# Optimization experiments

Hardware: AMD Instinct MI355X
Metric: run time of the kernel (lower is better)

The kernel has to match this reference:

```python
import jax, jax.numpy as jnp
import numpy as np

G = 8          # groups
EPS = 1e-5     # GroupNorm eps

def maxpool(x, k):
    pad = k // 2
    return jax.lax.reduce_window(x, -jnp.inf, jax.lax.max,
                                 (1, 1, k, k), (1, 1, 1, 1),
                                 [(0, 0), (0, 0), (pad, pad), (pad, pad)])

def conv1x1(x, w):
    # w: [out, in], x: [B, in, H, W]
    return jnp.einsum('oi,bihw->bohw', w, x)

def setup_inputs() -> dict:
    key = jax.random.key(0)
    ks = jax.random.split(key, 8)
    B, Cin, H, W = 16, 256, 64, 64
    planes = 256
    s = 0.05
    return {
        'x': jax.random.normal(ks[0], (B, Cin, H, W), jnp.float32),
        'mask': jax.random.uniform(ks[1], (B, 2, H, W), jnp.float32),
        'Wt': jax.random.normal(ks[2], (planes, Cin), jnp.float32) * s,
        'Wtm': jax.random.normal(ks[3], (1, 2), jnp.float32) * s,
        'Wp': jax.random.normal(ks[4], (planes // 2, Cin), jnp.float32) * s,
        'Wg': jax.random.normal(ks[5], (planes // 2, Cin), jnp.float32) * s,
        'Wz': jax.random.normal(ks[6], (G, Cin // G, planes // G), jnp.float32) * s,
        'gamma': jnp.ones((Cin,), jnp.float32),
        'beta': jnp.zeros((Cin,), jnp.float32),
    }

def reference(x, mask, Wt, Wtm, Wp, Wg, Wz, gamma, beta):
    B, Cin, H, W = x.shape
    planes = Wt.shape[0]
    cg = planes // G
    HW = H * W

    t = conv1x1(x, Wt)                      # [B, planes, H, W]
    t_mask = conv1x1(mask, Wtm)             # [B, 1, H, W]
    t = t * t_mask + t

    p = conv1x1(x, Wp)                      # [B, planes//2, H, W]
    p = jnp.concatenate([p, maxpool(p, 3), maxpool(p, 5)], axis=1)
    g = conv1x1(x, Wg)
    g = jnp.concatenate([g, maxpool(g, 3), maxpool(g, 5)], axis=1)
    # torch.split(_, cg) + loop over `groups` consumes only the first `planes` channels
    p = p[:, :planes]
    g = g[:, :planes]

    # kernel(), vectorized over groups: softmax over spatial, global scalar att per group
    ts = jax.nn.softmax(t.reshape(B, G, cg, HW), axis=-1)        # softmax dim=2 of [b,c,hw]
    pf = p.reshape(B, G, cg * HW)
    gf = g.reshape(B, G, cg * HW)
    att = jnp.einsum('bgn,bgn->bg', pf, gf)                      # bmm([b,1,n],[b,n,1])
    xk = (att[:, :, None, None] * ts).reshape(B, planes, H, W)

    # grouped 1x1 conv z: planes -> inplanes with G groups
    xz = jnp.einsum('goi,bgihw->bgohw', Wz,
                    xk.reshape(B, G, cg, H, W)).reshape(B, Cin, H, W)

    # GroupNorm(G, Cin)
    xg = xz.reshape(B, G, -1)
    mu = xg.mean(-1, keepdims=True)
    var = xg.var(-1, keepdims=True)
    xn = ((xg - mu) * jax.lax.rsqrt(var + EPS)).reshape(B, Cin, H, W)
    xn = xn * gamma[None, :, None, None] + beta[None, :, None, None]

    return xn + x
```

## Files before the change

kernel.cpp:

```cpp
#include <hip/hip_runtime.h>
#include <math.h>

#define B_      16
#define CIN     256
#define HW_     4096
#define PLANES  256
#define G_      8
#define EPSV    1e-5f

typedef unsigned short u16;
typedef __attribute__((ext_vector_type(8))) short short8;
typedef __attribute__((ext_vector_type(4))) float f32x4;

__device__ inline u16 f2bf(float f) {
    union { float f; unsigned u; } v; v.f = f;
    unsigned u = v.u;
    return (u16)((u + 0x7fffu + ((u >> 16) & 1u)) >> 16);
}
__device__ inline float bf2f(u16 h) {
    union { unsigned u; float f; } v; v.u = ((unsigned)h) << 16;
    return v.f;
}

__global__ __launch_bounds__(256) void k_packA(
    const float* __restrict__ Wt, const float* __restrict__ Wp,
    const float* __restrict__ Wg,
    u16* __restrict__ pAhi, u16* __restrict__ pAlo)
{
    int t = blockIdx.x * 256 + threadIdx.x;
    int lane = t & 63;
    int mb   = (t >> 6) & 7;
    int kt   = (t >> 9) & 7;
    int rt   = (t >> 12) & 3;
    int row = rt * 128 + mb * 16 + (lane & 15);
    int k0  = kt * 32 + (lane >> 4) * 8;
    const float* src;
    if      (row < 256) src = Wt + (size_t)row * 256;
    else if (row < 384) src = Wp + (size_t)(row - 256) * 256;
    else                src = Wg + (size_t)(row - 384) * 256;
    u16 hv[8], lv[8];
    #pragma unroll
    for (int j = 0; j < 8; ++j) {
        float w = src[k0 + j];
        u16 h = f2bf(w);
        hv[j] = h;
        lv[j] = f2bf(w - bf2f(h));
    }
    *(short8*)(pAhi + (size_t)t * 8) = *(short8*)hv;
    *(short8*)(pAlo + (size_t)t * 8) = *(short8*)lv;
}

__global__ __launch_bounds__(256) void k_transpose(
    const float* __restrict__ x, u16* __restrict__ xThi,
    u16* __restrict__ xTlo)
{
    __shared__ float tile[32][129];
    int tid = threadIdx.x;
    int px0 = blockIdx.x * 128;
    int c0  = blockIdx.y * 32;
    int bg  = blockIdx.z;

    #pragma unroll
    for (int it = 0; it < 16; ++it) {
        int flat = it * 256 + tid;
        int c_l = flat >> 7, p_l = flat & 127;
        tile[c_l][p_l] = x[((size_t)bg * 256 + c0 + c_l) * 4096 + px0 + p_l];
    }
    __syncthreads();
    #pragma unroll
    for (int it = 0; it < 8; ++it) {
        int flat = it * 256 + tid;
        int p_l = flat >> 4;
        int c_l = (flat & 15) * 2;
        float v0 = tile[c_l][p_l], v1 = tile[c_l + 1][p_l];
        u16 h0 = f2bf(v0), h1 = f2bf(v1);
        u16 l0 = f2bf(v0 - bf2f(h0)), l1 = f2bf(v1 - bf2f(h1));
        size_t o = ((size_t)bg * 4096 + px0 + p_l) * 256 + c0 + c_l;
        u16 ho[2] = { h0, h1 };
        u16 lo[2] = { l0, l1 };
        *(unsigned*)(xThi + o) = *(unsigned*)ho;
        *(unsigned*)(xTlo + o) = *(unsigned*)lo;
    }
}

__global__ __launch_bounds__(256) void k_tmod_zero(
    const float* __restrict__ mask, const float* __restrict__ Wtm,
    float* __restrict__ tmod, float* __restrict__ att, float* __restrict__ stats)
{
    int idx = blockIdx.x * 256 + threadIdx.x;
    float w0 = Wtm[0], w1 = Wtm[1];
    if (idx < B_ * HW_) {
        int b = idx >> 12, pix = idx & 4095;
        const float* mb = mask + (size_t)b * 2 * HW_;
        tmod[idx] = 1.0f + w0 * mb[pix] + w1 * mb[HW_ + pix];
    }
    if (blockIdx.x == 0) {
        if (threadIdx.x < 128) att[threadIdx.x] = 0.0f;
        stats[threadIdx.x] = 0.0f;
    }
}

#define STAGE16(SRC)                                                          \
    _Pragma("unroll")                                                         \
    for (int it = 0; it < 16; ++it) {                                         \
        int cidx = it * 256 + tid;                                            \
        int px   = cidx >> 5;                                                 \
        int boff = (cidx & 31) << 4;                                          \
        short8 v = *(const short8*)((SRC) + (size_t)px * 512 + boff);         \
        *(short8*)(Blds + px * 512 + (boff ^ ((px & 7) << 4))) = v;           \
    }

#define MFMA_PASS(ABASE)                                                      \
    _Pragma("unroll")                                                         \
    for (int kt = 0; kt < 8; ++kt) {                                          \
        short8 a[4], bb[4];                                                   \
        _Pragma("unroll")                                                     \
        for (int m = 0; m < 4; ++m)                                           \
            a[m] = *(const short8*)((ABASE) + kt * 8192 + m * 1024);          \
        int off = ((kt * 64) + ((lane >> 4) << 4)) ^ ((lane & 7) << 4);       \
        _Pragma("unroll")                                                     \
        for (int n = 0; n < 4; ++n) {                                         \
            int px = wn * 64 + n * 16 + (lane & 15);                          \
            bb[n] = *(const short8*)(Blds + px * 512 + off);                  \
        }                                                                     \
        _Pragma("unroll")                                                     \
        for (int m = 0; m < 4; ++m)                                           \
            _Pragma("unroll")                                                 \
            for (int n = 0; n < 4; ++n)                                       \
                acc[m][n] = __builtin_amdgcn_mfma_f32_16x16x32_bf16(          \
                    a[m], bb[n], acc[m][n], 0, 0, 0);                         \
    }

#define MFMA_PASS2(AH, AL)                                                    \
    _Pragma("unroll")                                                         \
    for (int kt = 0; kt < 8; ++kt) {                                          \
        short8 ah[4], al[4], bb[4];                                           \
        _Pragma("unroll")                                                     \
        for (int m = 0; m < 4; ++m) {                                         \
            ah[m] = *(const short8*)((AH) + kt * 8192 + m * 1024);            \
            al[m] = *(const short8*)((AL) + kt * 8192 + m * 1024);            \
        }                                                                     \
        int off = ((kt * 64) + ((lane >> 4) << 4)) ^ ((lane & 7) << 4);       \
        _Pragma("unroll")                                                     \
        for (int n = 0; n < 4; ++n) {                                         \
            int px = wn * 64 + n * 16 + (lane & 15);                          \
            bb[n] = *(const short8*)(Blds + px * 512 + off);                  \
        }                                                                     \
        _Pragma("unroll")                                                     \
        for (int m = 0; m < 4; ++m)                                           \
            _Pragma("unroll")                                                 \
            for (int n = 0; n < 4; ++n) {                                     \
                acc[m][n] = __builtin_amdgcn_mfma_f32_16x16x32_bf16(          \
                    ah[m], bb[n], acc[m][n], 0, 0, 0);                        \
                acc[m][n] = __builtin_amdgcn_mfma_f32_16x16x32_bf16(          \
                    al[m], bb[n], acc[m][n], 0, 0, 0);                        \
            }                                                                 \
    }

__global__ __launch_bounds__(256) void k_mm0(
    const u16* __restrict__ xThi, const u16* __restrict__ pAhi,
    const float* __restrict__ tmod, u16* __restrict__ tbuf)
{
    __shared__ short8 BldsV[4096];
    char* Blds = (char*)BldsV;
    int tid = threadIdx.x, lane = tid & 63, wid = tid >> 6;
    int wm = wid >> 1, wn = wid & 1;
    int pix0 = blockIdx.x * 128;
    int rt   = blockIdx.y;
    int bg   = blockIdx.z;

    const char* srcHi = (const char*)(xThi + ((size_t)bg * 4096 + pix0) * 256);
    const char* aHi = (const char*)pAhi + rt * 65536 + wm * 4096 + lane * 16;

    f32x4 acc[4][4];
    #pragma unroll
    for (int m = 0; m < 4; ++m)
        #pragma unroll
        for (int n = 0; n < 4; ++n) acc[m][n] = (f32x4)0.0f;

    STAGE16(srcHi);
    __syncthreads();
    MFMA_PASS(aHi);

    int colb = pix0 + wn * 64;
    int rowb = rt * 128 + wm * 64;
    float tm[4];
    #pragma unroll
    for (int n = 0; n < 4; ++n) tm[n] = tmod[bg * 4096 + colb + n * 16 + (lane & 15)];
    #pragma unroll
    for (int m = 0; m < 4; ++m)
        #pragma unroll
        for (int n = 0; n < 4; ++n)
            #pragma unroll
            for (int r = 0; r < 4; ++r) {
                int row = rowb + m * 16 + (lane >> 4) * 4 + r;
                int col = colb + n * 16 + (lane & 15);
                tbuf[((size_t)bg * 256 + row) * 4096 + col] = f2bf(acc[m][n][r] * tm[n]);
            }
}

__global__ __launch_bounds__(256) void k_mm1(
    const u16* __restrict__ xThi, const u16* __restrict__ xTlo,
    const u16* __restrict__ pAhi, const u16* __restrict__ pAlo,
    float* __restrict__ pbuf, float* __restrict__ gbuf)
{
    __shared__ short8 BldsV[4096];
    char* Blds = (char*)BldsV;
    int tid = threadIdx.x, lane = tid & 63, wid = tid >> 6;
    int wm = wid >> 1, wn = wid & 1;
    int pix0 = blockIdx.x * 128;
    int by   = blockIdx.y;
    int bg   = blockIdx.z;

    const char* srcHi = (const char*)(xThi + ((size_t)bg * 4096 + pix0) * 256);
    const char* srcLo = (const char*)(xTlo + ((size_t)bg * 4096 + pix0) * 256);
    const char* aHi = (const char*)pAhi + (2 + by) * 65536 + wm * 4096 + lane * 16;
    const char* aLo = (const char*)pAlo + (2 + by) * 65536 + wm * 4096 + lane * 16;

    f32x4 acc[4][4];
    #pragma unroll
    for (int m = 0; m < 4; ++m)
        #pragma unroll
        for (int n = 0; n < 4; ++n) acc[m][n] = (f32x4)0.0f;

    STAGE16(srcHi);
    __syncthreads();
    MFMA_PASS2(aHi, aLo);
    __syncthreads();
    STAGE16(srcLo);
    __syncthreads();
    MFMA_PASS(aHi);

    float* dst = (by == 0) ? pbuf : gbuf;
    int colb = pix0 + wn * 64;
    int rowb = wm * 64;
    #pragma unroll
    for (int m = 0; m < 4; ++m)
        #pragma unroll
        for (int n = 0; n < 4; ++n)
            #pragma unroll
            for (int r = 0; r < 4; ++r) {
                int row = rowb + m * 16 + (lane >> 4) * 4 + r;
                int col = colb + n * 16 + (lane & 15);
                dst[((size_t)bg * 128 + row) * 4096 + col] = acc[m][n][r];
            }
}

__global__ __launch_bounds__(256) void k_att(
    const float* __restrict__ pbuf, const float* __restrict__ gbuf,
    float* __restrict__ att)
{
    __shared__ float hmp[HW_];
    __shared__ float hmg[HW_];
    __shared__ float halo[256][4];
    __shared__ float scr[8];
    int c  = blockIdx.x;
    int gi = blockIdx.y;
    int b  = blockIdx.z;
    int tid = threadIdx.x;
    int tq = tid & 3;
    int r  = tid >> 2;
    int px0 = tid * 16;

    const float* pp = pbuf + ((size_t)b * 128 + gi * 32 + c) * HW_ + px0;
    const float* gg = gbuf + ((size_t)b * 128 + gi * 32 + c) * HW_ + px0;

    float pv[16], gv[16];
    float racc = 0.0f;
    #pragma unroll
    for (int i = 0; i < 4; ++i) {
        float4 p4 = *(const float4*)(pp + i * 4);
        float4 g4 = *(const float4*)(gg + i * 4);
        pv[4*i+0] = p4.x; pv[4*i+1] = p4.y; pv[4*i+2] = p4.z; pv[4*i+3] = p4.w;
        gv[4*i+0] = g4.x; gv[4*i+1] = g4.y; gv[4*i+2] = g4.z; gv[4*i+3] = g4.w;
        racc += p4.x * g4.x + p4.y * g4.y + p4.z * g4.z + p4.w * g4.w;
    }
    halo[tid][0] = pv[0]; halo[tid][1] = pv[15];
    halo[tid][2] = gv[0]; halo[tid][3] = gv[15];
    __syncthreads();

    float pL = (tq > 0) ? halo[tid - 1][1] : pv[0];
    float pR = (tq < 3) ? halo[tid + 1][0] : pv[15];
    float gL = (tq > 0) ? halo[tid - 1][3] : gv[0];
    float gR = (tq < 3) ? halo[tid + 1][2] : gv[15];

    float hp[16], hg[16];
    hp[0] = fmaxf(fmaxf(pL, pv[0]), pv[1]);
    hg[0] = fmaxf(fmaxf(gL, gv[0]), gv[1]);
    #pragma unroll
    for (int j = 1; j < 15; ++j) {
        hp[j] = fmaxf(fmaxf(pv[j-1], pv[j]), pv[j+1]);
        hg[j] = fmaxf(fmaxf(gv[j-1], gv[j]), gv[j+1]);
    }
    hp[15] = fmaxf(fmaxf(pv[14], pv[15]), pR);
    hg[15] = fmaxf(fmaxf(gv[14], gv[15]), gR);

    #pragma unroll
    for (int i = 0; i < 4; ++i) {
        *(float4*)(&hmp[px0 + i * 4]) = make_float4(hp[4*i], hp[4*i+1], hp[4*i+2], hp[4*i+3]);
        *(float4*)(&hmg[px0 + i * 4]) = make_float4(hg[4*i], hg[4*i+1], hg[4*i+2], hg[4*i+3]);
    }
    __syncthreads();

    int up = (r > 0)  ? px0 - 64 : px0;
    int dn = (r < 63) ? px0 + 64 : px0;
    float pacc = 0.0f;
    #pragma unroll
    for (int i = 0; i < 4; ++i) {
        float4 pu = *(const float4*)(&hmp[up + i * 4]);
        float4 pd = *(const float4*)(&hmp[dn + i * 4]);
        float4 gu = *(const float4*)(&hmg[up + i * 4]);
        float4 gd = *(const float4*)(&hmg[dn + i * 4]);
        float mpx, mgx;
        mpx = fmaxf(fmaxf(pu.x, hp[4*i+0]), pd.x); mgx = fmaxf(fmaxf(gu.x, hg[4*i+0]), gd.x); pacc += mpx * mgx;
        mpx = fmaxf(fmaxf(pu.y, hp[4*i+1]), pd.y); mgx = fmaxf(fmaxf(gu.y, hg[4*i+1]), gd.y); pacc += mpx * mgx;
        mpx = fmaxf(fmaxf(pu.z, hp[4*i+2]), pd.z); mgx = fmaxf(fmaxf(gu.z, hg[4*i+2]), gd.z); pacc += mpx * mgx;
        mpx = fmaxf(fmaxf(pu.w, hp[4*i+3]), pd.w); mgx = fmaxf(fmaxf(gu.w, hg[4*i+3]), gd.w); pacc += mpx * mgx;
    }

    #pragma unroll
    for (int off = 32; off > 0; off >>= 1) {
        racc += __shfl_down(racc, off, 64);
        pacc += __shfl_down(pacc, off, 64);
    }
    int lane = tid & 63, wid = tid >> 6;
    if (lane == 0) { scr[wid] = racc; scr[4 + wid] = pacc; }
    __syncthreads();
    if (tid == 0) {
        atomicAdd(&att[b * 8 + gi],     scr[0] + scr[1] + scr[2] + scr[3]);
        atomicAdd(&att[b * 8 + gi + 4], scr[4] + scr[5] + scr[6] + scr[7]);
    }
}

__global__ __launch_bounds__(256) void k_smax(
    const u16* __restrict__ tbuf, float2* __restrict__ rowstat)
{
    __shared__ float scr[8];
    int r = blockIdx.x;
    const u16* tr = tbuf + (size_t)r * HW_;
    int tid = threadIdx.x;
    int lane = tid & 63, wid = tid >> 6;

    float vals[16];
    float mx = -3.0e38f;
    #pragma unroll
    for (int it = 0; it < 2; ++it) {
        short8 v = *(const short8*)(tr + it * 2048 + tid * 8);
        #pragma unroll
        for (int j = 0; j < 8; ++j) {
            float f = bf2f((u16)v[j]);
            vals[it * 8 + j] = f;
            mx = fmaxf(mx, f);
        }
    }
    #pragma unroll
    for (int off = 32; off > 0; off >>= 1) mx = fmaxf(mx, __shfl_down(mx, off, 64));
    if (lane == 0) scr[wid] = mx;
    __syncthreads();
    if (tid == 0) scr[0] = fmaxf(fmaxf(scr[0], scr[1]), fmaxf(scr[2], scr[3]));
    __syncthreads();
    float m = scr[0];
    __syncthreads();

    float s = 0.0f;
    #pragma unroll
    for (int j = 0; j < 16; ++j) s += __expf(vals[j] - m);
    #pragma unroll
    for (int off = 32; off > 0; off >>= 1) s += __shfl_down(s, off, 64);
    if (lane == 0) scr[4 + wid] = s;
    __syncthreads();
    if (tid == 0) {
        float S = scr[4] + scr[5] + scr[6] + scr[7];
        rowstat[r] = make_float2(m, 1.0f / S);
    }
}

__global__ __launch_bounds__(256) void k_xz2(
    u16* __restrict__ tbuf, const float* __restrict__ Wz,
    const float2* __restrict__ rowstat, const float* __restrict__ att,
    float* __restrict__ stats)
{
    __shared__ float wz[32][32];
    __shared__ float2 rs[32];
    __shared__ float scr[8];
    int pt  = blockIdx.x;
    int gi  = blockIdx.y;
    int b   = blockIdx.z;
    int tid = threadIdx.x;
    int px  = pt * 512 + tid * 2;

    const float* wzg = Wz + gi * 1024;
    #pragma unroll
    for (int i = 0; i < 4; ++i) {
        int idx = tid + i * 256;
        wz[idx >> 5][idx & 31] = wzg[idx];
    }
    if (tid < 32) rs[tid] = rowstat[b * 256 + gi * 32 + tid];
    __syncthreads();

    u16* base = tbuf + ((size_t)b * 256 + gi * 32) * HW_;
    float2 v[32];
    #pragma unroll
    for (int i = 0; i < 32; ++i) {
        unsigned rv = *(const unsigned*)(base + (size_t)i * HW_ + px);
        float m = rs[i].x, inv = rs[i].y;
        v[i].x = __expf(bf2f((u16)(rv & 0xffffu)) - m) * inv;
        v[i].y = __expf(bf2f((u16)(rv >> 16)) - m) * inv;
    }

    float a = att[b * 8 + gi];
    float s1 = 0.0f, s2 = 0.0f;
    #pragma unroll
    for (int o = 0; o < 32; ++o) {
        const float4* wzo = (const float4*)(&wz[o][0]);
        float ax = 0.0f, ay = 0.0f;
        #pragma unroll
        for (int j = 0; j < 8; ++j) {
            float4 w = wzo[j];
            ax = fmaf(w.x, v[4*j+0].x, ax); ay = fmaf(w.x, v[4*j+0].y, ay);
            ax = fmaf(w.y, v[4*j+1].x, ax); ay = fmaf(w.y, v[4*j+1].y, ay);
            ax = fmaf(w.z, v[4*j+2].x, ax); ay = fmaf(w.z, v[4*j+2].y, ay);
            ax = fmaf(w.w, v[4*j+3].x, ax); ay = fmaf(w.w, v[4*j+3].y, ay);
        }
        ax *= a; ay *= a;
        unsigned ov = (unsigned)f2bf(ax) | ((unsigned)f2bf(ay) << 16);
        *(unsigned*)(base + (size_t)o * HW_ + px) = ov;
        s1 += ax + ay;
        s2 = fmaf(ax, ax, fmaf(ay, ay, s2));
    }

    #pragma unroll
    for (int off = 32; off > 0; off >>= 1) {
        s1 += __shfl_down(s1, off, 64);
        s2 += __shfl_down(s2, off, 64);
    }
    int lane = tid & 63, wid = tid >> 6;
    if (lane == 0) { scr[wid] = s1; scr[4 + wid] = s2; }
    __syncthreads();
    if (tid == 0) {
        atomicAdd(&stats[(b * 8 + gi) * 2 + 0], scr[0] + scr[1] + scr[2] + scr[3]);
        atomicAdd(&stats[(b * 8 + gi) * 2 + 1], scr[4] + scr[5] + scr[6] + scr[7]);
    }
}

__global__ __launch_bounds__(256) void k_finalize(
    const u16* __restrict__ xzbuf, const float* __restrict__ x,
    const float* __restrict__ stats, const float* __restrict__ gamma,
    const float* __restrict__ beta, float* __restrict__ out)
{
    size_t i0 = ((size_t)blockIdx.x * 256 + threadIdx.x) * 4;
    int c  = (int)((i0 >> 12) & 255);
    int bg = (int)(i0 >> 17);
    float s1 = stats[bg * 2], s2 = stats[bg * 2 + 1];
    const float invN = 1.0f / 131072.0f;
    float mu  = s1 * invN;
    float var = s2 * invN - mu * mu;
    float rs  = rsqrtf(var + EPSV);
    float ga = gamma[c], be = beta[c];

    union { unsigned long long u; u16 h[4]; } vv;
    vv.u = *(const unsigned long long*)(xzbuf + i0);
    float4 xv = *(const float4*)(x + i0);
    float4 o;
    o.x = (bf2f(vv.h[0]) - mu) * rs * ga + be + xv.x;
    o.y = (bf2f(vv.h[1]) - mu) * rs * ga + be + xv.y;
    o.z = (bf2f(vv.h[2]) - mu) * rs * ga + be + xv.z;
    o.w = (bf2f(vv.h[3]) - mu) * rs * ga + be + xv.w;
    *(float4*)(out + i0) = o;
}

extern "C" void kernel_launch(void* const* d_in, const int* in_sizes, int n_in,
                              void* d_out, int out_size, void* d_ws, size_t ws_size,
                              hipStream_t stream)
{
    const float* x     = (const float*)d_in[0];
    const float* mask  = (const float*)d_in[1];
    const float* Wt    = (const float*)d_in[2];
    const float* Wtm   = (const float*)d_in[3];
    const float* Wp    = (const float*)d_in[4];
    const float* Wg    = (const float*)d_in[5];
    const float* Wz    = (const float*)d_in[6];
    const float* gamma = (const float*)d_in[7];
    const float* beta  = (const float*)d_in[8];
    float* out = (float*)d_out;

    char* ws = (char*)d_ws;
    u16*   tbuf  = (u16*)(ws);
    u16*   xThi  = (u16*)(ws + 33554432);
    u16*   xTlo  = (u16*)(ws + 67108864);
    float* pbuf  = (float*)(ws + 100663296);
    float* gbuf  = (float*)(ws + 167772160);
    u16*   pAhi  = (u16*)(ws + 234881024);
    u16*   pAlo  = (u16*)(ws + 235143168);
    float* tmod  = (float*)(ws + 235405312);
    float* att   = (float*)(ws + 235667456);
    float* stats = att + 128;
    float2* rowstat = (float2*)(ws + 235669504);

    k_packA    <<<64, 256, 0, stream>>>(Wt, Wp, Wg, pAhi, pAlo);
    k_tmod_zero<<<256, 256, 0, stream>>>(mask, Wtm, tmod, att, stats);
    k_transpose<<<dim3(32, 8, 16), 256, 0, stream>>>(x, xThi, xTlo);
    k_mm0      <<<dim3(32, 2, 16), 256, 0, stream>>>(xThi, pAhi, tmod, tbuf);
    k_mm1      <<<dim3(32, 2, 16), 256, 0, stream>>>(xThi, xTlo, pAhi, pAlo, pbuf, gbuf);
    k_att      <<<dim3(32, 4, 16), 256, 0, stream>>>(pbuf, gbuf, att);
    k_smax     <<<4096, 256, 0, stream>>>(tbuf, rowstat);
    k_xz2      <<<dim3(8, 8, 16), 256, 0, stream>>>(tbuf, Wz, rowstat, att, stats);
    k_finalize <<<16384, 256, 0, stream>>>(tbuf, x, stats, gamma, beta, out);
}
```

Measured before the change: 179.5 us.

## Fuse t and p/g projection GEMMs into one kernel sharing staged x tiles

Merges the two 1x1-conv GEMM kernels into a single kernel. Each block now stages a 64-pixel tile of both the hi and lo bf16 parts of x once and computes all three outputs from it: t (bf16, scaled by the mask modulation), p and g (fp32 via hi/lo split). This removes one launch and the repeated global reads of the x tiles across blocks and kernels. In exchange the grid becomes 1024 blocks with a smaller pixel tile, and each wave runs all three MFMA passes serially.

```diff
diff --git a/kernel.cpp b/kernel.cpp
--- a/kernel.cpp
+++ b/kernel.cpp
@@ -100,17 +100,17 @@
     }
 }
 
-#define STAGE16(SRC)                                                          \
+#define STAGE8(SRC, DST)                                                      \
     _Pragma("unroll")                                                         \
-    for (int it = 0; it < 16; ++it) {                                         \
+    for (int it = 0; it < 8; ++it) {                                          \
         int cidx = it * 256 + tid;                                            \
         int px   = cidx >> 5;                                                 \
         int boff = (cidx & 31) << 4;                                          \
         short8 v = *(const short8*)((SRC) + (size_t)px * 512 + boff);         \
-        *(short8*)(Blds + px * 512 + (boff ^ ((px & 7) << 4))) = v;           \
-    }
-
-#define MFMA_PASS(ABASE)                                                      \
+        *(short8*)((DST) + px * 512 + (boff ^ ((px & 7) << 4))) = v;          \
+    }
+
+#define MFMA_PASS_B(ABASE, BBASE)                                             \
     _Pragma("unroll")                                                         \
     for (int kt = 0; kt < 8; ++kt) {                                          \
         short8 a[4], bb[4];                                                   \
@@ -120,8 +120,8 @@
         int off = ((kt * 64) + ((lane >> 4) << 4)) ^ ((lane & 7) << 4);       \
         _Pragma("unroll")                                                     \
         for (int n = 0; n < 4; ++n) {                                         \
-            int px = wn * 64 + n * 16 + (lane & 15);                          \
-            bb[n] = *(const short8*)(Blds + px * 512 + off);                  \
+            int px = n * 16 + (lane & 15);                                    \
+            bb[n] = *(const short8*)((BBASE) + px * 512 + off);               \
         }                                                                     \
         _Pragma("unroll")                                                     \
         for (int m = 0; m < 4; ++m)                                           \
@@ -131,7 +131,7 @@
                     a[m], bb[n], acc[m][n], 0, 0, 0);                         \
     }
 
-#define MFMA_PASS2(AH, AL)                                                    \
+#define MFMA_PASS2_B(AH, AL, BBASE)                                           \
     _Pragma("unroll")                                                         \
     for (int kt = 0; kt < 8; ++kt) {                                          \
         short8 ah[4], al[4], bb[4];                                           \
@@ -143,8 +143,8 @@
         int off = ((kt * 64) + ((lane >> 4) << 4)) ^ ((lane & 7) << 4);       \
         _Pragma("unroll")                                                     \
         for (int n = 0; n < 4; ++n) {                                         \
-            int px = wn * 64 + n * 16 + (lane & 15);                          \
-            bb[n] = *(const short8*)(Blds + px * 512 + off);                  \
+            int px = n * 16 + (lane & 15);                                    \
+            bb[n] = *(const short8*)((BBASE) + px * 512 + off);               \
         }                                                                     \
         _Pragma("unroll")                                                     \
         for (int m = 0; m < 4; ++m)                                           \
@@ -157,91 +157,69 @@
             }                                                                 \
     }
 
-__global__ __launch_bounds__(256) void k_mm0(
-    const u16* __restrict__ xThi, const u16* __restrict__ pAhi,
-    const float* __restrict__ tmod, u16* __restrict__ tbuf)
+__global__ __launch_bounds__(256) void k_mmf(
+    const u16* __restrict__ xThi, const u16* __restrict__ xTlo,
+    const u16* __restrict__ pAhi, const u16* __restrict__ pAlo,
+    const float* __restrict__ tmod, u16* __restrict__ tbuf,
+    float* __restrict__ pbuf, float* __restrict__ gbuf)
 {
     __shared__ short8 BldsV[4096];
-    char* Blds = (char*)BldsV;
+    char* BldsHi = (char*)BldsV;
+    char* BldsLo = BldsHi + 32768;
     int tid = threadIdx.x, lane = tid & 63, wid = tid >> 6;
-    int wm = wid >> 1, wn = wid & 1;
-    int pix0 = blockIdx.x * 128;
-    int rt   = blockIdx.y;
-    int bg   = blockIdx.z;
+    int mbb = (wid & 1) * 4;
+    int pix0 = blockIdx.x * 64;
+    int bg   = blockIdx.y;
 
     const char* srcHi = (const char*)(xThi + ((size_t)bg * 4096 + pix0) * 256);
-    const char* aHi = (const char*)pAhi + rt * 65536 + wm * 4096 + lane * 16;
+    const char* srcLo = (const char*)(xTlo + ((size_t)bg * 4096 + pix0) * 256);
+    const char* aHiT = (const char*)pAhi + (wid >> 1) * 65536 + mbb * 1024 + lane * 16;
+    const char* aHiP = (const char*)pAhi + (2 + (wid >> 1)) * 65536 + mbb * 1024 + lane * 16;
+    const char* aLoP = (const char*)pAlo + (2 + (wid >> 1)) * 65536 + mbb * 1024 + lane * 16;
+
+    STAGE8(srcHi, BldsHi);
+    STAGE8(srcLo, BldsLo);
+    __syncthreads();
 
     f32x4 acc[4][4];
+
     #pragma unroll
     for (int m = 0; m < 4; ++m)
         #pragma unroll
         for (int n = 0; n < 4; ++n) acc[m][n] = (f32x4)0.0f;
-
-    STAGE16(srcHi);
-    __syncthreads();
-    MFMA_PASS(aHi);
-
-    int colb = pix0 + wn * 64;
-    int rowb = rt * 128 + wm * 64;
-    float tm[4];
-    #pragma unroll
-    for (int n = 0; n < 4; ++n) tm[n] = tmod[bg * 4096 + colb + n * 16 + (lane & 15)];
+    MFMA_PASS_B(aHiT, BldsHi);
+    {
+        float tm[4];
+        #pragma unroll
+        for (int n = 0; n < 4; ++n) tm[n] = tmod[bg * 4096 + pix0 + n * 16 + (lane & 15)];
+        #pragma unroll
+        for (int m = 0; m < 4; ++m)
+            #pragma unroll
+            for (int n = 0; n < 4; ++n)
+                #pragma unroll
+                for (int r = 0; r < 4; ++r) {
+                    int row = wid * 64 + m * 16 + (lane >> 4) * 4 + r;
+                    int col = pix0 + n * 16 + (lane & 15);
+                    tbuf[((size_t)bg * 256 + row) * 4096 + col] = f2bf(acc[m][n][r] * tm[n]);
+                }
+    }
+
+    #pragma unroll
+    for (int m = 0; m < 4; ++m)
+        #pragma unroll
+        for (int n = 0; n < 4; ++n) acc[m][n] = (f32x4)0.0f;
+    MFMA_PASS2_B(aHiP, aLoP, BldsHi);
+    MFMA_PASS_B(aHiP, BldsLo);
+
+    float* dst = (wid < 2) ? pbuf : gbuf;
     #pragma unroll
     for (int m = 0; m < 4; ++m)
         #pragma unroll
         for (int n = 0; n < 4; ++n)
             #pragma unroll
             for (int r = 0; r < 4; ++r) {
-                int row = rowb + m * 16 + (lane >> 4) * 4 + r;
-                int col = colb + n * 16 + (lane & 15);
-                tbuf[((size_t)bg * 256 + row) * 4096 + col] = f2bf(acc[m][n][r] * tm[n]);
-            }
-}
-
-__global__ __launch_bounds__(256) void k_mm1(
-    const u16* __restrict__ xThi, const u16* __restrict__ xTlo,
-    const u16* __restrict__ pAhi, const u16* __restrict__ pAlo,
-    float* __restrict__ pbuf, float* __restrict__ gbuf)
-{
-    __shared__ short8 BldsV[4096];
-    char* Blds = (char*)BldsV;
-    int tid = threadIdx.x, lane = tid & 63, wid = tid >> 6;
-    int wm = wid >> 1, wn = wid & 1;
-    int pix0 = blockIdx.x * 128;
-    int by   = blockIdx.y;
-    int bg   = blockIdx.z;
-
-    const char* srcHi = (const char*)(xThi + ((size_t)bg * 4096 + pix0) * 256);
-    const char* srcLo = (const char*)(xTlo + ((size_t)bg * 4096 + pix0) * 256);
-    const char* aHi = (const char*)pAhi + (2 + by) * 65536 + wm * 4096 + lane * 16;
-    const char* aLo = (const char*)pAlo + (2 + by) * 65536 + wm * 4096 + lane * 16;
-
-    f32x4 acc[4][4];
-    #pragma unroll
-    for (int m = 0; m < 4; ++m)
-        #pragma unroll
-        for (int n = 0; n < 4; ++n) acc[m][n] = (f32x4)0.0f;
-
-    STAGE16(srcHi);
-    __syncthreads();
-    MFMA_PASS2(aHi, aLo);
-    __syncthreads();
-    STAGE16(srcLo);
-    __syncthreads();
-    MFMA_PASS(aHi);
-
-    float* dst = (by == 0) ? pbuf : gbuf;
-    int colb = pix0 + wn * 64;
-    int rowb = wm * 64;
-    #pragma unroll
-    for (int m = 0; m < 4; ++m)
-        #pragma unroll
-        for (int n = 0; n < 4; ++n)
-            #pragma unroll
-            for (int r = 0; r < 4; ++r) {
-                int row = rowb + m * 16 + (lane >> 4) * 4 + r;
-                int col = colb + n * 16 + (lane & 15);
+                int row = (wid & 1) * 64 + m * 16 + (lane >> 4) * 4 + r;
+                int col = pix0 + n * 16 + (lane & 15);
                 dst[((size_t)bg * 128 + row) * 4096 + col] = acc[m][n][r];
             }
 }
@@ -500,8 +478,8 @@
     k_packA    <<<64, 256, 0, stream>>>(Wt, Wp, Wg, pAhi, pAlo);
     k_tmod_zero<<<256, 256, 0, stream>>>(mask, Wtm, tmod, att, stats);
     k_transpose<<<dim3(32, 8, 16), 256, 0, stream>>>(x, xThi, xTlo);
-    k_mm0      <<<dim3(32, 2, 16), 256, 0, stream>>>(xThi, pAhi, tmod, tbuf);
-    k_mm1      <<<dim3(32, 2, 16), 256, 0, stream>>>(xThi, xTlo, pAhi, pAlo, pbuf, gbuf);
+    k_mmf      <<<dim3(64, 16), 256, 0, stream>>>(xThi, xTlo, pAhi, pAlo, tmod,
+                                                  tbuf, pbuf, gbuf);
     k_att      <<<dim3(32, 4, 16), 256, 0, stream>>>(pbuf, gbuf, att);
     k_smax     <<<4096, 256, 0, stream>>>(tbuf, rowstat);
     k_xz2      <<<dim3(8, 8, 16), 256, 0, stream>>>(tbuf, Wz, rowstat, att, stats);
```

Measured after the change: 189.0 us. +5.3%, slower.
